# Kernel tuning notes

Hardware: AMD Instinct MI355X
Metric: run time of the kernel (lower is better)

## Reference

```python
import jax, jax.numpy as jnp
import numpy as np

N_NODES = 100000
N_EDGES = 1600000
NFEAT, NHID, NCLASS = 512, 128, 40


def setup_inputs() -> dict:
    key = jax.random.key(0)
    ks = jax.random.split(key, 8)
    features = jax.random.normal(ks[0], (N_NODES, NFEAT), dtype=jnp.float32)
    edge_src = jax.random.randint(ks[1], (N_EDGES,), 0, N_NODES, dtype=jnp.int32)
    edge_dst = jax.random.randint(ks[2], (N_EDGES,), 0, N_NODES, dtype=jnp.int32)
    edge_weight = jax.random.uniform(ks[3], (N_EDGES,), dtype=jnp.float32)
    W1 = jax.random.normal(ks[4], (NFEAT, NHID), dtype=jnp.float32) * (1.0 / np.sqrt(NFEAT))
    b1 = jnp.zeros((NHID,), dtype=jnp.float32)
    W2 = jax.random.normal(ks[5], (NHID, NCLASS), dtype=jnp.float32) * (1.0 / np.sqrt(NHID))
    b2 = jnp.zeros((NCLASS,), dtype=jnp.float32)
    return {"features": features, "edge_src": edge_src, "edge_dst": edge_dst,
            "edge_weight": edge_weight, "W1": W1, "b1": b1, "W2": W2, "b2": b2}


def _gcn_conv(x, W, b, edge_src, edge_dst, edge_weight, num_nodes):
    # GCNconv: adj @ (x @ W) + b, adj given as weighted edge list (spmm).
    h = x @ W                                   # [N, out]
    msgs = edge_weight[:, None] * h[edge_src]   # [E, out] gather + scale
    agg = jax.ops.segment_sum(msgs, edge_dst, num_segments=num_nodes)  # [N, out]
    return agg + b


def reference(features, edge_src, edge_dst, edge_weight, W1, b1, W2, b2):
    x = _gcn_conv(features, W1, b1, edge_src, edge_dst, edge_weight, N_NODES)
    x = jax.nn.relu(x)
    # dropout is identity in eval mode (deterministic reference)
    x = _gcn_conv(x, W2, b2, edge_src, edge_dst, edge_weight, N_NODES)
    return jax.nn.log_softmax(x, axis=1)
```

## Files before the change

kernel.cpp:

```cpp
#include <hip/hip_runtime.h>
#include <hip/hip_bf16.h>
#include <math.h>

#define N_NODES 100000
#define N_EDGES 1600000
#define NFEAT 512
#define NHID 128
#define NCLASS 40

#define BSH 7
#define BNODES (1 << BSH)
#define NBUCK ((N_NODES + BNODES - 1) / BNODES)

#define PCHUNK 4096
#define PEPT 16
#define PNB ((N_EDGES + PCHUNK - 1) / PCHUNK)

#define CAP 2560
#define KSTG 10

typedef short bf16x8 __attribute__((ext_vector_type(8)));
typedef float f32x4 __attribute__((ext_vector_type(4)));

static __device__ __forceinline__ unsigned short f32_to_bf16(float f) {
    unsigned int u = __float_as_uint(f);
    unsigned int r = u + 0x7FFFu + ((u >> 16) & 1u);
    return (unsigned short)(r >> 16);
}
static __device__ __forceinline__ float bf16_to_f32(unsigned short h) {
    return __uint_as_float(((unsigned int)h) << 16);
}

__global__ __launch_bounds__(256) void bucket_hist_transpose_kernel(
    const int* __restrict__ dst, int* __restrict__ histG,
    const float* __restrict__ W1, unsigned short* __restrict__ Wt,
    const float* __restrict__ W2, unsigned short* __restrict__ W2t, int E)
{
    const int blk = blockIdx.x;
    if (blk >= PNB + 256) {
        int i = (blk - PNB - 256) * 256 + threadIdx.x;
        if (i < 48 * 128) {
            int c = i >> 7;
            int k = i & 127;
            W2t[i] = (c < NCLASS) ? f32_to_bf16(W2[k * NCLASS + c]) : 0;
        }
        return;
    }
    if (blk >= PNB) {
        int tid2 = (blk - PNB) * 256 + threadIdx.x;
        int n = tid2 >> 9;
        int k = tid2 & 511;
        Wt[tid2] = f32_to_bf16(W1[k * NHID + n]);
        return;
    }
    __shared__ int hl[NBUCK];
    const int t = threadIdx.x;
    for (int j = t; j < NBUCK; j += 256) hl[j] = 0;
    __syncthreads();
    const int c0 = blk * PCHUNK;
    #pragma unroll
    for (int i = 0; i < PEPT; i++) {
        int e = c0 + t + i * 256;
        if (e < E) atomicAdd(&hl[dst[e] >> BSH], 1);
    }
    __syncthreads();
    for (int j = t; j < NBUCK; j += 256) {
        int c = hl[j];
        if (c) atomicAdd(&histG[j * 16], c);
    }
}

__global__ __launch_bounds__(1024) void bucket_scan_kernel(
    const int* __restrict__ histG, int* __restrict__ bofs,
    int* __restrict__ bcursor)
{
    __shared__ int sh[1024];
    const int t = threadIdx.x;
    int v = (t < NBUCK) ? histG[t * 16] : 0;
    sh[t] = v;
    __syncthreads();
    #pragma unroll
    for (int off = 1; off < 1024; off <<= 1) {
        int u = (t >= off) ? sh[t - off] : 0;
        __syncthreads();
        sh[t] += u;
        __syncthreads();
    }
    if (t < NBUCK) {
        int excl = sh[t] - v;
        bofs[t] = excl;
        bcursor[t] = excl;
    }
    if (t == NBUCK - 1) bofs[NBUCK] = sh[t];
}

__global__ __launch_bounds__(256) void partition_kernel(
    const int* __restrict__ src, const int* __restrict__ dst,
    const float* __restrict__ w, int* __restrict__ bcursor,
    int2* __restrict__ sortedA, int E)
{
    __shared__ int hist[NBUCK];
    __shared__ int bbase[NBUCK];
    const int t = threadIdx.x;
    const int c0 = blockIdx.x * PCHUNK;

    for (int j = t; j < NBUCK; j += 256) hist[j] = 0;
    __syncthreads();

    int  myb[PEPT];
    int2 myv[PEPT];
    #pragma unroll
    for (int i = 0; i < PEPT; i++) {
        int e = c0 + t + i * 256;
        if (e < E) {
            int d = dst[e];
            myb[i] = d >> BSH;
            myv[i] = make_int2(src[e] | ((d & (BNODES - 1)) << 17),
                               __float_as_int(w[e]));
            atomicAdd(&hist[myb[i]], 1);
        } else {
            myb[i] = -1;
        }
    }
    __syncthreads();

    for (int j = t; j < NBUCK; j += 256) {
        int c = hist[j];
        bbase[j] = c ? atomicAdd(&bcursor[j], c) : 0;
    }
    __syncthreads();

    #pragma unroll
    for (int i = 0; i < PEPT; i++) {
        if (myb[i] >= 0) {
            int p = atomicAdd(&bbase[myb[i]], 1);
            sortedA[p] = myv[i];
        }
    }
}

__global__ __launch_bounds__(256) void gemm1_mfma_kernel(
    const float* __restrict__ A,
    const unsigned short* __restrict__ Wt,
    unsigned short* __restrict__ h1b,
    int M)
{
    __shared__ unsigned short cstage[4][32 * 130];

    const int tid = threadIdx.x;
    const int w = tid >> 6;
    const int lane = tid & 63;
    const int lr = lane & 15;
    const int quad = lane >> 4;
    const int m0 = blockIdx.x * 128 + w * 32;

    f32x4 acc[2][8];
    #pragma unroll
    for (int rt = 0; rt < 2; rt++)
        #pragma unroll
        for (int ct = 0; ct < 8; ct++)
            acc[rt][ct] = (f32x4){0.f, 0.f, 0.f, 0.f};

    int r0 = m0 + lr;
    int r1 = m0 + 16 + lr;
    int r0c = r0 < M ? r0 : M - 1;
    int r1c = r1 < M ? r1 : M - 1;
    const float* a0p = A + (size_t)r0c * NFEAT + quad * 8;
    const float* a1p = A + (size_t)r1c * NFEAT + quad * 8;
    const unsigned short* bp = Wt + (size_t)lr * NFEAT + quad * 8;

    #pragma unroll 2
    for (int k0 = 0; k0 < NFEAT; k0 += 32) {
        float4 a0a = *(const float4*)(a0p + k0);
        float4 a0b = *(const float4*)(a0p + k0 + 4);
        float4 a1a = *(const float4*)(a1p + k0);
        float4 a1b = *(const float4*)(a1p + k0 + 4);

        bf16x8 fb[8];
        #pragma unroll
        for (int ct = 0; ct < 8; ct++)
            fb[ct] = *(const bf16x8*)(bp + (size_t)ct * 16 * NFEAT + k0);

        bf16x8 fa0, fa1;
        fa0[0] = (short)f32_to_bf16(a0a.x); fa0[1] = (short)f32_to_bf16(a0a.y);
        fa0[2] = (short)f32_to_bf16(a0a.z); fa0[3] = (short)f32_to_bf16(a0a.w);
        fa0[4] = (short)f32_to_bf16(a0b.x); fa0[5] = (short)f32_to_bf16(a0b.y);
        fa0[6] = (short)f32_to_bf16(a0b.z); fa0[7] = (short)f32_to_bf16(a0b.w);
        fa1[0] = (short)f32_to_bf16(a1a.x); fa1[1] = (short)f32_to_bf16(a1a.y);
        fa1[2] = (short)f32_to_bf16(a1a.z); fa1[3] = (short)f32_to_bf16(a1a.w);
        fa1[4] = (short)f32_to_bf16(a1b.x); fa1[5] = (short)f32_to_bf16(a1b.y);
        fa1[6] = (short)f32_to_bf16(a1b.z); fa1[7] = (short)f32_to_bf16(a1b.w);

        #pragma unroll
        for (int ct = 0; ct < 8; ct++) {
            acc[0][ct] = __builtin_amdgcn_mfma_f32_16x16x32_bf16(fa0, fb[ct], acc[0][ct], 0, 0, 0);
            acc[1][ct] = __builtin_amdgcn_mfma_f32_16x16x32_bf16(fa1, fb[ct], acc[1][ct], 0, 0, 0);
        }
    }

    unsigned short* st = cstage[w];
    #pragma unroll
    for (int rt = 0; rt < 2; rt++)
        #pragma unroll
        for (int ct = 0; ct < 8; ct++)
            #pragma unroll
            for (int i = 0; i < 4; i++) {
                int row = rt * 16 + quad * 4 + i;
                int col = ct * 16 + lr;
                st[row * 130 + col] = f32_to_bf16(acc[rt][ct][i]);
            }

    #pragma unroll
    for (int g = 0; g < 8; g++) {
        int row = g * 4 + (lane >> 4);
        int c8 = lane & 15;
        const unsigned short* rp = &st[row * 130 + c8 * 8];
        uint4 v = *(const uint4*)rp;
        int gr = m0 + row;
        if (gr < M)
            *(uint4*)&h1b[(size_t)gr * NHID + c8 * 8] = v;
    }
}

__global__ __launch_bounds__(256) void agg1_gemm2_kernel(
    const int2* __restrict__ sortedA, const int* __restrict__ bofs,
    const unsigned short* __restrict__ h1b, const float* __restrict__ b1,
    const unsigned short* __restrict__ W2t, float* __restrict__ h2, int N)
{
    __shared__ __align__(16) int2 ebuf[CAP];
    __shared__ __align__(16) unsigned short xs[128][136];
    __shared__ __align__(16) unsigned short wt2s[48 * 136];
    __shared__ int ncnt[BNODES];
    __shared__ int nofs[BNODES];
    __shared__ int ncur[BNODES];
    __shared__ int sc[BNODES];
    __shared__ float b1s[128];

    const int tid = threadIdx.x;
    const int b = blockIdx.x;
    const int node0 = b << BSH;
    const int nn = min(BNODES, N - node0);
    const int beg = bofs[b];
    const int end = bofs[b + 1];
    const int cnt = end - beg;
    const bool fits = (cnt <= CAP);

    for (int i = tid; i < 48 * 128; i += 256)
        wt2s[(i >> 7) * 136 + (i & 127)] = W2t[i];
    if (tid < 128) {
        b1s[tid] = b1[tid];
        ncnt[tid] = 0;
    }
    __syncthreads();

    int2 myrec[KSTG];
    if (fits) {
        #pragma unroll
        for (int k = 0; k < KSTG; k++) {
            int i = tid + k * 256;
            if (i < cnt) {
                int2 r = sortedA[beg + i];
                myrec[k] = r;
                atomicAdd(&ncnt[(r.x >> 17) & 127], 1);
            }
        }
        __syncthreads();
        if (tid < 128) sc[tid] = ncnt[tid];
        __syncthreads();
        #pragma unroll
        for (int off = 1; off < 128; off <<= 1) {
            int u = (tid < 128 && tid >= off) ? sc[tid - off] : 0;
            __syncthreads();
            if (tid < 128) sc[tid] += u;
            __syncthreads();
        }
        if (tid < 128) {
            int e0 = sc[tid] - ncnt[tid];
            nofs[tid] = e0;
            ncur[tid] = e0;
        }
        __syncthreads();
        #pragma unroll
        for (int k = 0; k < KSTG; k++) {
            int i = tid + k * 256;
            if (i < cnt) {
                int nd = (myrec[k].x >> 17) & 127;
                int p = atomicAdd(&ncur[nd], 1);
                ebuf[p] = myrec[k];
            }
        }
        __syncthreads();
    }

    const int g = tid >> 5;
    const int lane = tid & 31;
    const unsigned short* hb = h1b + lane * 4;

    for (int ln = g * 16; ln < g * 16 + 16; ln++) {
        if (ln >= nn) break;
        float4 acc = {0.f, 0.f, 0.f, 0.f};
        if (fits) {
            const int s0 = nofs[ln];
            const int c0 = ncnt[ln];
            int j = 0;
            for (; j + 8 <= c0; j += 8) {
                int2 r[8];
                #pragma unroll
                for (int q = 0; q < 8; q++) r[q] = ebuf[s0 + j + q];
                ushort4 hv[8];
                #pragma unroll
                for (int q = 0; q < 8; q++)
                    hv[q] = *(const ushort4*)(hb + (size_t)(r[q].x & 0x1FFFF) * NHID);
                #pragma unroll
                for (int q = 0; q < 8; q++) {
                    float wj = __int_as_float(r[q].y);
                    acc.x = fmaf(wj, bf16_to_f32(hv[q].x), acc.x);
                    acc.y = fmaf(wj, bf16_to_f32(hv[q].y), acc.y);
                    acc.z = fmaf(wj, bf16_to_f32(hv[q].z), acc.z);
                    acc.w = fmaf(wj, bf16_to_f32(hv[q].w), acc.w);
                }
            }
            for (; j + 4 <= c0; j += 4) {
                int2 r[4];
                #pragma unroll
                for (int q = 0; q < 4; q++) r[q] = ebuf[s0 + j + q];
                ushort4 hv[4];
                #pragma unroll
                for (int q = 0; q < 4; q++)
                    hv[q] = *(const ushort4*)(hb + (size_t)(r[q].x & 0x1FFFF) * NHID);
                #pragma unroll
                for (int q = 0; q < 4; q++) {
                    float wj = __int_as_float(r[q].y);
                    acc.x = fmaf(wj, bf16_to_f32(hv[q].x), acc.x);
                    acc.y = fmaf(wj, bf16_to_f32(hv[q].y), acc.y);
                    acc.z = fmaf(wj, bf16_to_f32(hv[q].z), acc.z);
                    acc.w = fmaf(wj, bf16_to_f32(hv[q].w), acc.w);
                }
            }
            for (; j < c0; j++) {
                int2 r = ebuf[s0 + j];
                float wj = __int_as_float(r.y);
                ushort4 hv = *(const ushort4*)(hb + (size_t)(r.x & 0x1FFFF) * NHID);
                acc.x = fmaf(wj, bf16_to_f32(hv.x), acc.x);
                acc.y = fmaf(wj, bf16_to_f32(hv.y), acc.y);
                acc.z = fmaf(wj, bf16_to_f32(hv.z), acc.z);
                acc.w = fmaf(wj, bf16_to_f32(hv.w), acc.w);
            }
        } else {
            for (int e = beg; e < end; e++) {
                int2 r = sortedA[e];
                if (((r.x >> 17) & 127) == ln) {
                    float wj = __int_as_float(r.y);
                    ushort4 hv = *(const ushort4*)(hb + (size_t)(r.x & 0x1FFFF) * NHID);
                    acc.x = fmaf(wj, bf16_to_f32(hv.x), acc.x);
                    acc.y = fmaf(wj, bf16_to_f32(hv.y), acc.y);
                    acc.z = fmaf(wj, bf16_to_f32(hv.z), acc.z);
                    acc.w = fmaf(wj, bf16_to_f32(hv.w), acc.w);
                }
            }
        }
        float4 bb = *(const float4*)&b1s[lane * 4];
        ushort4 px;
        px.x = f32_to_bf16(fmaxf(acc.x + bb.x, 0.f));
        px.y = f32_to_bf16(fmaxf(acc.y + bb.y, 0.f));
        px.z = f32_to_bf16(fmaxf(acc.z + bb.z, 0.f));
        px.w = f32_to_bf16(fmaxf(acc.w + bb.w, 0.f));
        *(ushort4*)&xs[ln][lane * 4] = px;
    }
    __syncthreads();

    const int wv = tid >> 6;
    const int l64 = tid & 63;
    const int lr = l64 & 15;
    const int quad = l64 >> 4;

    f32x4 c_[2][3];
    #pragma unroll
    for (int mt = 0; mt < 2; mt++)
        #pragma unroll
        for (int nt = 0; nt < 3; nt++)
            c_[mt][nt] = (f32x4){0.f, 0.f, 0.f, 0.f};

    #pragma unroll
    for (int k0 = 0; k0 < 128; k0 += 32) {
        bf16x8 af[2], bf_[3];
        #pragma unroll
        for (int mt = 0; mt < 2; mt++)
            af[mt] = *(const bf16x8*)&xs[wv * 32 + mt * 16 + lr][k0 + quad * 8];
        #pragma unroll
        for (int nt = 0; nt < 3; nt++)
            bf_[nt] = *(const bf16x8*)&wt2s[(nt * 16 + lr) * 136 + k0 + quad * 8];
        #pragma unroll
        for (int mt = 0; mt < 2; mt++)
            #pragma unroll
            for (int nt = 0; nt < 3; nt++)
                c_[mt][nt] = __builtin_amdgcn_mfma_f32_16x16x32_bf16(
                    af[mt], bf_[nt], c_[mt][nt], 0, 0, 0);
    }

    #pragma unroll
    for (int mt = 0; mt < 2; mt++)
        #pragma unroll
        for (int nt = 0; nt < 3; nt++) {
            int col = nt * 16 + lr;
            if (col < NCLASS) {
                #pragma unroll
                for (int i = 0; i < 4; i++) {
                    int row = wv * 32 + mt * 16 + quad * 4 + i;
                    if (row < nn)
                        h2[(size_t)(node0 + row) * NCLASS + col] = c_[mt][nt][i];
                }
            }
        }
}

__global__ __launch_bounds__(256) void agg2_softmax_kernel(
    const int2* __restrict__ sortedA, const int* __restrict__ bofs,
    const float* __restrict__ h2, const float* __restrict__ b2,
    float* __restrict__ out, int N)
{
    __shared__ __align__(16) int2 ebuf[CAP];
    __shared__ int ncnt[BNODES];
    __shared__ int nofs[BNODES];
    __shared__ int ncur[BNODES];
    __shared__ int sc[BNODES];

    const int tid = threadIdx.x;
    const int b = blockIdx.x;
    const int node0 = b << BSH;
    const int nn = min(BNODES, N - node0);
    const int beg = bofs[b];
    const int end = bofs[b + 1];
    const int cnt = end - beg;
    const bool fits = (cnt <= CAP);

    for (int i = tid; i < BNODES; i += 256) ncnt[i] = 0;
    __syncthreads();

    int2 myrec[KSTG];
    if (fits) {
        #pragma unroll
        for (int k = 0; k < KSTG; k++) {
            int i = tid + k * 256;
            if (i < cnt) {
                int2 r = sortedA[beg + i];
                myrec[k] = r;
                atomicAdd(&ncnt[(r.x >> 17) & 127], 1);
            }
        }
        __syncthreads();
        if (tid < 128) sc[tid] = ncnt[tid];
        __syncthreads();
        #pragma unroll
        for (int off = 1; off < 128; off <<= 1) {
            int u = (tid < 128 && tid >= off) ? sc[tid - off] : 0;
            __syncthreads();
            if (tid < 128) sc[tid] += u;
            __syncthreads();
        }
        if (tid < 128) {
            int e0 = sc[tid] - ncnt[tid];
            nofs[tid] = e0;
            ncur[tid] = e0;
        }
        __syncthreads();
        #pragma unroll
        for (int k = 0; k < KSTG; k++) {
            int i = tid + k * 256;
            if (i < cnt) {
                int nd = (myrec[k].x >> 17) & 127;
                int p = atomicAdd(&ncur[nd], 1);
                ebuf[p] = myrec[k];
            }
        }
        __syncthreads();
    }

    const int grp = tid >> 4;
    const int l16 = tid & 15;
    const float* hp0 = h2 + l16 * 4;

    for (int it = 0; it < 8; it++) {
        const int ln = it * 16 + grp;
        float4 acc = {0.f, 0.f, 0.f, 0.f};
        if (ln < nn) {
            if (fits) {
                const int s0 = nofs[ln];
                const int c0 = ncnt[ln];
                int j = 0;
                for (; j + 8 <= c0; j += 8) {
                    int2 r[8];
                    #pragma unroll
                    for (int q = 0; q < 8; q++) r[q] = ebuf[s0 + j + q];
                    if (l16 < 10) {
                        float4 v[8];
                        #pragma unroll
                        for (int q = 0; q < 8; q++)
                            v[q] = *(const float4*)(hp0 + (size_t)(r[q].x & 0x1FFFF) * NCLASS);
                        #pragma unroll
                        for (int q = 0; q < 8; q++) {
                            float wj = __int_as_float(r[q].y);
                            acc.x = fmaf(wj, v[q].x, acc.x);
                            acc.y = fmaf(wj, v[q].y, acc.y);
                            acc.z = fmaf(wj, v[q].z, acc.z);
                            acc.w = fmaf(wj, v[q].w, acc.w);
                        }
                    }
                }
                for (; j + 4 <= c0; j += 4) {
                    int2 r[4];
                    #pragma unroll
                    for (int q = 0; q < 4; q++) r[q] = ebuf[s0 + j + q];
                    if (l16 < 10) {
                        float4 v[4];
                        #pragma unroll
                        for (int q = 0; q < 4; q++)
                            v[q] = *(const float4*)(hp0 + (size_t)(r[q].x & 0x1FFFF) * NCLASS);
                        #pragma unroll
                        for (int q = 0; q < 4; q++) {
                            float wj = __int_as_float(r[q].y);
                            acc.x = fmaf(wj, v[q].x, acc.x);
                            acc.y = fmaf(wj, v[q].y, acc.y);
                            acc.z = fmaf(wj, v[q].z, acc.z);
                            acc.w = fmaf(wj, v[q].w, acc.w);
                        }
                    }
                }
                for (; j < c0; j++) {
                    int2 r = ebuf[s0 + j];
                    if (l16 < 10) {
                        float wj = __int_as_float(r.y);
                        float4 v = *(const float4*)(hp0 + (size_t)(r.x & 0x1FFFF) * NCLASS);
                        acc.x = fmaf(wj, v.x, acc.x);
                        acc.y = fmaf(wj, v.y, acc.y);
                        acc.z = fmaf(wj, v.z, acc.z);
                        acc.w = fmaf(wj, v.w, acc.w);
                    }
                }
            } else {
                for (int e = beg; e < end; e++) {
                    int2 r = sortedA[e];
                    if (((r.x >> 17) & 127) == ln && l16 < 10) {
                        float wj = __int_as_float(r.y);
                        float4 v = *(const float4*)(hp0 + (size_t)(r.x & 0x1FFFF) * NCLASS);
                        acc.x = fmaf(wj, v.x, acc.x);
                        acc.y = fmaf(wj, v.y, acc.y);
                        acc.z = fmaf(wj, v.z, acc.z);
                        acc.w = fmaf(wj, v.w, acc.w);
                    }
                }
            }
        }
        bool act = (ln < nn) && (l16 < 10);
        float mx = -INFINITY;
        if (act) {
            float4 bb = *(const float4*)&b2[l16 * 4];
            acc.x += bb.x; acc.y += bb.y; acc.z += bb.z; acc.w += bb.w;
            mx = fmaxf(fmaxf(acc.x, acc.y), fmaxf(acc.z, acc.w));
        }
        #pragma unroll
        for (int o = 8; o > 0; o >>= 1) mx = fmaxf(mx, __shfl_xor(mx, o, 16));
        float sm = act ? expf(acc.x - mx) + expf(acc.y - mx) +
                         expf(acc.z - mx) + expf(acc.w - mx) : 0.f;
        #pragma unroll
        for (int o = 8; o > 0; o >>= 1) sm += __shfl_xor(sm, o, 16);
        if (act) {
            float l = mx + logf(sm);
            float4 o4 = {acc.x - l, acc.y - l, acc.z - l, acc.w - l};
            *(float4*)&out[(size_t)(node0 + ln) * NCLASS + l16 * 4] = o4;
        }
    }
}

extern "C" void kernel_launch(void* const* d_in, const int* in_sizes, int n_in,
                              void* d_out, int out_size, void* d_ws, size_t ws_size,
                              hipStream_t stream) {
    const float* features = (const float*)d_in[0];
    const int* edge_src   = (const int*)d_in[1];
    const int* edge_dst   = (const int*)d_in[2];
    const float* edge_w   = (const float*)d_in[3];
    const float* W1       = (const float*)d_in[4];
    const float* b1       = (const float*)d_in[5];
    const float* W2       = (const float*)d_in[6];
    const float* b2       = (const float*)d_in[7];
    float* out = (float*)d_out;

    char* base = (char*)d_ws;
    float*          h2       = (float*)base;
    unsigned short* h1b      = (unsigned short*)(base + 51200000);
    unsigned short* Wt       = (unsigned short*)(base + 76800000);
    int*            histG    = (int*)(base + 76931072);
    int*            bofs     = (int*)(base + 77000000);
    int*            bcursor  = (int*)(base + 77010000);
    unsigned short* W2t      = (unsigned short*)(base + 77020000);
    int2*           sortedA  = (int2*)(base + 90540000);

    hipMemsetAsync(histG, 0, NBUCK * 16 * sizeof(int), stream);

    bucket_hist_transpose_kernel<<<PNB + 256 + 24, 256, 0, stream>>>(
        edge_dst, histG, W1, Wt, W2, W2t, N_EDGES);
    bucket_scan_kernel<<<1, 1024, 0, stream>>>(histG, bofs, bcursor);
    partition_kernel<<<PNB, 256, 0, stream>>>(
        edge_src, edge_dst, edge_w, bcursor, sortedA, N_EDGES);

    gemm1_mfma_kernel<<<(N_NODES + 127) / 128, 256, 0, stream>>>(features, Wt, h1b, N_NODES);

    agg1_gemm2_kernel<<<NBUCK, 256, 0, stream>>>(
        sortedA, bofs, h1b, b1, W2t, h2, N_NODES);

    agg2_softmax_kernel<<<NBUCK, 256, 0, stream>>>(
        sortedA, bofs, h2, b2, out, N_NODES);
}
```

Measured before the change: 544.9 us.

## Halve bucket size and fuse edge partition with GEMM1 in one launch

Buckets shrink from 128 to 64 nodes, which doubles the number of aggregation blocks for better occupancy and smaller per-block shared memory. The scan now handles two buckets per thread to cover the larger bucket count. The edge partition and the feature GEMM are merged into one heterogeneous launch so the atomic-heavy partition blocks overlap with the MFMA blocks, and the partition now re-reads dst instead of holding edge records in registers. Risks include more global cursor atomics, W2 being reloaded by twice as many blocks, and less reuse in the GEMM2 tile.

```diff
diff --git a/kernel.cpp b/kernel.cpp
--- a/kernel.cpp
+++ b/kernel.cpp
@@ -8,7 +8,7 @@
 #define NHID 128
 #define NCLASS 40
 
-#define BSH 7
+#define BSH 6
 #define BNODES (1 << BSH)
 #define NBUCK ((N_NODES + BNODES - 1) / BNODES)
 
@@ -16,8 +16,12 @@
 #define PEPT 16
 #define PNB ((N_EDGES + PCHUNK - 1) / PCHUNK)
 
-#define CAP 2560
-#define KSTG 10
+#define PCHUNK2 8192
+#define FPNB ((N_EDGES + PCHUNK2 - 1) / PCHUNK2)
+#define GEMM1_NB ((N_NODES + 127) / 128)
+
+#define CAP 1536
+#define KSTG 6
 
 typedef short bf16x8 __attribute__((ext_vector_type(8)));
 typedef float f32x4 __attribute__((ext_vector_type(4)));
@@ -76,8 +80,11 @@
 {
     __shared__ int sh[1024];
     const int t = threadIdx.x;
-    int v = (t < NBUCK) ? histG[t * 16] : 0;
-    sh[t] = v;
+    const int i0 = 2 * t, i1 = 2 * t + 1;
+    int v0 = (i0 < NBUCK) ? histG[i0 * 16] : 0;
+    int v1 = (i1 < NBUCK) ? histG[i1 * 16] : 0;
+    int s = v0 + v1;
+    sh[t] = s;
     __syncthreads();
     #pragma unroll
     for (int off = 1; off < 1024; off <<= 1) {
@@ -86,73 +93,64 @@
         sh[t] += u;
         __syncthreads();
     }
-    if (t < NBUCK) {
-        int excl = sh[t] - v;
-        bofs[t] = excl;
-        bcursor[t] = excl;
-    }
-    if (t == NBUCK - 1) bofs[NBUCK] = sh[t];
-}
-
-__global__ __launch_bounds__(256) void partition_kernel(
-    const int* __restrict__ src, const int* __restrict__ dst,
+    int base = sh[t] - s;
+    if (i0 < NBUCK) { bofs[i0] = base;      bcursor[i0] = base; }
+    if (i1 < NBUCK) { bofs[i1] = base + v0; bcursor[i1] = base + v0; }
+    if (t == 1023) bofs[NBUCK] = sh[1023];
+}
+
+__global__ __launch_bounds__(256) void partition_gemm1_kernel(
+    const int* __restrict__ src, const int* __restrict__ dstp,
     const float* __restrict__ w, int* __restrict__ bcursor,
-    int2* __restrict__ sortedA, int E)
+    int2* __restrict__ sortedA,
+    const float* __restrict__ A, const unsigned short* __restrict__ Wt,
+    unsigned short* __restrict__ h1b, int E, int M)
 {
-    __shared__ int hist[NBUCK];
-    __shared__ int bbase[NBUCK];
-    const int t = threadIdx.x;
-    const int c0 = blockIdx.x * PCHUNK;
-
-    for (int j = t; j < NBUCK; j += 256) hist[j] = 0;
-    __syncthreads();
-
-    int  myb[PEPT];
-    int2 myv[PEPT];
-    #pragma unroll
-    for (int i = 0; i < PEPT; i++) {
-        int e = c0 + t + i * 256;
-        if (e < E) {
-            int d = dst[e];
-            myb[i] = d >> BSH;
-            myv[i] = make_int2(src[e] | ((d & (BNODES - 1)) << 17),
-                               __float_as_int(w[e]));
-            atomicAdd(&hist[myb[i]], 1);
-        } else {
-            myb[i] = -1;
-        }
-    }
-    __syncthreads();
-
-    for (int j = t; j < NBUCK; j += 256) {
-        int c = hist[j];
-        bbase[j] = c ? atomicAdd(&bcursor[j], c) : 0;
-    }
-    __syncthreads();
-
-    #pragma unroll
-    for (int i = 0; i < PEPT; i++) {
-        if (myb[i] >= 0) {
-            int p = atomicAdd(&bbase[myb[i]], 1);
-            sortedA[p] = myv[i];
-        }
-    }
-}
-
-__global__ __launch_bounds__(256) void gemm1_mfma_kernel(
-    const float* __restrict__ A,
-    const unsigned short* __restrict__ Wt,
-    unsigned short* __restrict__ h1b,
-    int M)
-{
-    __shared__ unsigned short cstage[4][32 * 130];
+    __shared__ __align__(16) char smem[4 * 32 * 130 * 2];
 
     const int tid = threadIdx.x;
-    const int w = tid >> 6;
+
+    if (blockIdx.x < FPNB) {
+        int* hist  = (int*)smem;
+        int* bbase = hist + NBUCK;
+        const int c0 = blockIdx.x * PCHUNK2;
+
+        for (int j = tid; j < NBUCK; j += 256) hist[j] = 0;
+        __syncthreads();
+
+        #pragma unroll
+        for (int i = 0; i < PCHUNK2 / 256; i++) {
+            int e = c0 + tid + i * 256;
+            if (e < E) atomicAdd(&hist[dstp[e] >> BSH], 1);
+        }
+        __syncthreads();
+
+        for (int j = tid; j < NBUCK; j += 256) {
+            int c = hist[j];
+            bbase[j] = c ? atomicAdd(&bcursor[j], c) : 0;
+        }
+        __syncthreads();
+
+        #pragma unroll
+        for (int i = 0; i < PCHUNK2 / 256; i++) {
+            int e = c0 + tid + i * 256;
+            if (e < E) {
+                int d = dstp[e];
+                int p = atomicAdd(&bbase[d >> BSH], 1);
+                sortedA[p] = make_int2(src[e] | ((d & (BNODES - 1)) << 17),
+                                       __float_as_int(w[e]));
+            }
+        }
+        return;
+    }
+
+    unsigned short (*cstage)[32 * 130] = (unsigned short (*)[32 * 130])smem;
+
+    const int w4 = tid >> 6;
     const int lane = tid & 63;
     const int lr = lane & 15;
     const int quad = lane >> 4;
-    const int m0 = blockIdx.x * 128 + w * 32;
+    const int m0 = (blockIdx.x - FPNB) * 128 + w4 * 32;
 
     f32x4 acc[2][8];
     #pragma unroll
@@ -198,7 +196,7 @@
         }
     }
 
-    unsigned short* st = cstage[w];
+    unsigned short* st = cstage[w4];
     #pragma unroll
     for (int rt = 0; rt < 2; rt++)
         #pragma unroll
@@ -228,7 +226,7 @@
     const unsigned short* __restrict__ W2t, float* __restrict__ h2, int N)
 {
     __shared__ __align__(16) int2 ebuf[CAP];
-    __shared__ __align__(16) unsigned short xs[128][136];
+    __shared__ __align__(16) unsigned short xs[64][136];
     __shared__ __align__(16) unsigned short wt2s[48 * 136];
     __shared__ int ncnt[BNODES];
     __shared__ int nofs[BNODES];
@@ -247,10 +245,8 @@
 
     for (int i = tid; i < 48 * 128; i += 256)
         wt2s[(i >> 7) * 136 + (i & 127)] = W2t[i];
-    if (tid < 128) {
-        b1s[tid] = b1[tid];
-        ncnt[tid] = 0;
-    }
+    if (tid < 128) b1s[tid] = b1[tid];
+    if (tid < BNODES) ncnt[tid] = 0;
     __syncthreads();
 
     int2 myrec[KSTG];
@@ -261,20 +257,20 @@
             if (i < cnt) {
                 int2 r = sortedA[beg + i];
                 myrec[k] = r;
-                atomicAdd(&ncnt[(r.x >> 17) & 127], 1);
-            }
-        }
-        __syncthreads();
-        if (tid < 128) sc[tid] = ncnt[tid];
-        __syncthreads();
-        #pragma unroll
-        for (int off = 1; off < 128; off <<= 1) {
-            int u = (tid < 128 && tid >= off) ? sc[tid - off] : 0;
+                atomicAdd(&ncnt[(r.x >> 17) & (BNODES - 1)], 1);
+            }
+        }
+        __syncthreads();
+        if (tid < BNODES) sc[tid] = ncnt[tid];
+        __syncthreads();
+        #pragma unroll
+        for (int off = 1; off < BNODES; off <<= 1) {
+            int u = (tid < BNODES && tid >= off) ? sc[tid - off] : 0;
             __syncthreads();
-            if (tid < 128) sc[tid] += u;
+            if (tid < BNODES) sc[tid] += u;
             __syncthreads();
         }
-        if (tid < 128) {
+        if (tid < BNODES) {
             int e0 = sc[tid] - ncnt[tid];
             nofs[tid] = e0;
             ncur[tid] = e0;
@@ -284,7 +280,7 @@
         for (int k = 0; k < KSTG; k++) {
             int i = tid + k * 256;
             if (i < cnt) {
-                int nd = (myrec[k].x >> 17) & 127;
+                int nd = (myrec[k].x >> 17) & (BNODES - 1);
                 int p = atomicAdd(&ncur[nd], 1);
                 ebuf[p] = myrec[k];
             }
@@ -296,7 +292,7 @@
     const int lane = tid & 31;
     const unsigned short* hb = h1b + lane * 4;
 
-    for (int ln = g * 16; ln < g * 16 + 16; ln++) {
+    for (int ln = g * 8; ln < g * 8 + 8; ln++) {
         if (ln >= nn) break;
         float4 acc = {0.f, 0.f, 0.f, 0.f};
         if (fits) {
@@ -349,7 +345,7 @@
         } else {
             for (int e = beg; e < end; e++) {
                 int2 r = sortedA[e];
-                if (((r.x >> 17) & 127) == ln) {
+                if (((r.x >> 17) & (BNODES - 1)) == ln) {
                     float wj = __int_as_float(r.y);
                     ushort4 hv = *(const ushort4*)(hb + (size_t)(r.x & 0x1FFFF) * NHID);
                     acc.x = fmaf(wj, bf16_to_f32(hv.x), acc.x);
@@ -374,44 +370,36 @@
     const int lr = l64 & 15;
     const int quad = l64 >> 4;
 
-    f32x4 c_[2][3];
-    #pragma unroll
-    for (int mt = 0; mt < 2; mt++)
-        #pragma unroll
-        for (int nt = 0; nt < 3; nt++)
-            c_[mt][nt] = (f32x4){0.f, 0.f, 0.f, 0.f};
+    f32x4 c_[3];
+    #pragma unroll
+    for (int nt = 0; nt < 3; nt++)
+        c_[nt] = (f32x4){0.f, 0.f, 0.f, 0.f};
 
     #pragma unroll
     for (int k0 = 0; k0 < 128; k0 += 32) {
-        bf16x8 af[2], bf_[3];
-        #pragma unroll
-        for (int mt = 0; mt < 2; mt++)
-            af[mt] = *(const bf16x8*)&xs[wv * 32 + mt * 16 + lr][k0 + quad * 8];
+        bf16x8 af = *(const bf16x8*)&xs[wv * 16 + lr][k0 + quad * 8];
+        bf16x8 bf_[3];
         #pragma unroll
         for (int nt = 0; nt < 3; nt++)
             bf_[nt] = *(const bf16x8*)&wt2s[(nt * 16 + lr) * 136 + k0 + quad * 8];
         #pragma unroll
-        for (int mt = 0; mt < 2; mt++)
+        for (int nt = 0; nt < 3; nt++)
+            c_[nt] = __builtin_amdgcn_mfma_f32_16x16x32_bf16(
+                af, bf_[nt], c_[nt], 0, 0, 0);
+    }
+
+    #pragma unroll
+    for (int nt = 0; nt < 3; nt++) {
+        int col = nt * 16 + lr;
+        if (col < NCLASS) {
             #pragma unroll
-            for (int nt = 0; nt < 3; nt++)
-                c_[mt][nt] = __builtin_amdgcn_mfma_f32_16x16x32_bf16(
-                    af[mt], bf_[nt], c_[mt][nt], 0, 0, 0);
-    }
-
-    #pragma unroll
-    for (int mt = 0; mt < 2; mt++)
-        #pragma unroll
-        for (int nt = 0; nt < 3; nt++) {
-            int col = nt * 16 + lr;
-            if (col < NCLASS) {
-                #pragma unroll
-                for (int i = 0; i < 4; i++) {
-                    int row = wv * 32 + mt * 16 + quad * 4 + i;
-                    if (row < nn)
-                        h2[(size_t)(node0 + row) * NCLASS + col] = c_[mt][nt][i];
-                }
-            }
-        }
+            for (int i = 0; i < 4; i++) {
+                int row = wv * 16 + quad * 4 + i;
+                if (row < nn)
+                    h2[(size_t)(node0 + row) * NCLASS + col] = c_[nt][i];
+            }
+        }
+    }
 }
 
 __global__ __launch_bounds__(256) void agg2_softmax_kernel(
@@ -434,7 +422,7 @@
     const int cnt = end - beg;
     const bool fits = (cnt <= CAP);
 
-    for (int i = tid; i < BNODES; i += 256) ncnt[i] = 0;
+    if (tid < BNODES) ncnt[tid] = 0;
     __syncthreads();
 
     int2 myrec[KSTG];
@@ -445,20 +433,20 @@
             if (i < cnt) {
                 int2 r = sortedA[beg + i];
                 myrec[k] = r;
-                atomicAdd(&ncnt[(r.x >> 17) & 127], 1);
-            }
-        }
-        __syncthreads();
-        if (tid < 128) sc[tid] = ncnt[tid];
-        __syncthreads();
-        #pragma unroll
-        for (int off = 1; off < 128; off <<= 1) {
-            int u = (tid < 128 && tid >= off) ? sc[tid - off] : 0;
+                atomicAdd(&ncnt[(r.x >> 17) & (BNODES - 1)], 1);
+            }
+        }
+        __syncthreads();
+        if (tid < BNODES) sc[tid] = ncnt[tid];
+        __syncthreads();
+        #pragma unroll
+        for (int off = 1; off < BNODES; off <<= 1) {
+            int u = (tid < BNODES && tid >= off) ? sc[tid - off] : 0;
             __syncthreads();
-            if (tid < 128) sc[tid] += u;
+            if (tid < BNODES) sc[tid] += u;
             __syncthreads();
         }
-        if (tid < 128) {
+        if (tid < BNODES) {
             int e0 = sc[tid] - ncnt[tid];
             nofs[tid] = e0;
             ncur[tid] = e0;
@@ -468,7 +456,7 @@
         for (int k = 0; k < KSTG; k++) {
             int i = tid + k * 256;
             if (i < cnt) {
-                int nd = (myrec[k].x >> 17) & 127;
+                int nd = (myrec[k].x >> 17) & (BNODES - 1);
                 int p = atomicAdd(&ncur[nd], 1);
                 ebuf[p] = myrec[k];
             }
@@ -480,7 +468,7 @@
     const int l16 = tid & 15;
     const float* hp0 = h2 + l16 * 4;
 
-    for (int it = 0; it < 8; it++) {
+    for (int it = 0; it < 4; it++) {
         const int ln = it * 16 + grp;
         float4 acc = {0.f, 0.f, 0.f, 0.f};
         if (ln < nn) {
@@ -540,7 +528,7 @@
             } else {
                 for (int e = beg; e < end; e++) {
                     int2 r = sortedA[e];
-                    if (((r.x >> 17) & 127) == ln && l16 < 10) {
+                    if (((r.x >> 17) & (BNODES - 1)) == ln && l16 < 10) {
                         float wj = __int_as_float(r.y);
                         float4 v = *(const float4*)(hp0 + (size_t)(r.x & 0x1FFFF) * NCLASS);
                         acc.x = fmaf(wj, v.x, acc.x);
@@ -590,9 +578,9 @@
     unsigned short* h1b      = (unsigned short*)(base + 51200000);
     unsigned short* Wt       = (unsigned short*)(base + 76800000);
     int*            histG    = (int*)(base + 76931072);
-    int*            bofs     = (int*)(base + 77000000);
-    int*            bcursor  = (int*)(base + 77010000);
-    unsigned short* W2t      = (unsigned short*)(base + 77020000);
+    int*            bofs     = (int*)(base + 77040000);
+    int*            bcursor  = (int*)(base + 77050000);
+    unsigned short* W2t      = (unsigned short*)(base + 77060000);
     int2*           sortedA  = (int2*)(base + 90540000);
 
     hipMemsetAsync(histG, 0, NBUCK * 16 * sizeof(int), stream);
@@ -600,10 +588,10 @@
     bucket_hist_transpose_kernel<<<PNB + 256 + 24, 256, 0, stream>>>(
         edge_dst, histG, W1, Wt, W2, W2t, N_EDGES);
     bucket_scan_kernel<<<1, 1024, 0, stream>>>(histG, bofs, bcursor);
-    partition_kernel<<<PNB, 256, 0, stream>>>(
-        edge_src, edge_dst, edge_w, bcursor, sortedA, N_EDGES);
-
-    gemm1_mfma_kernel<<<(N_NODES + 127) / 128, 256, 0, stream>>>(features, Wt, h1b, N_NODES);
+
+    partition_gemm1_kernel<<<FPNB + GEMM1_NB, 256, 0, stream>>>(
+        edge_src, edge_dst, edge_w, bcursor, sortedA,
+        features, Wt, h1b, N_EDGES, N_NODES);
 
     agg1_gemm2_kernel<<<NBUCK, 256, 0, stream>>>(
         sortedA, bofs, h1b, b1, W2t, h2, N_NODES);
```

New measurement: 533.7 us. 2.1% less time.
